# Optimization experiments

Measured on AMD Instinct MI355X. Metric: run time of the kernel, lower is better.

The kernel has to match this reference:

```python
import jax, jax.numpy as jnp
import numpy as np

L, D, H, DK, FF, R, N, B = 8, 256, 8, 32, 1024, 37, 1024, 1
EPS = 1e-6


def setup_inputs() -> dict:
    key = jax.random.key(0)
    ks = jax.random.split(key, 16)
    def w(i, shape, s=0.05):
        return jax.random.normal(ks[i], shape, jnp.float32) * s
    return {
        "x": jax.random.normal(ks[0], (B, N, D), jnp.float32),
        "relations": jax.random.randint(ks[1], (N, N), 0, R),
        "Wq": w(2, (L, D, D)), "bq": jnp.zeros((L, D), jnp.float32),
        "Wk": w(3, (L, D, D)), "bk": jnp.zeros((L, D), jnp.float32),
        "Wv": w(4, (L, D, D)), "bv": jnp.zeros((L, D), jnp.float32),
        "Wo": w(5, (L, D, D)), "bo": jnp.zeros((L, D), jnp.float32),
        "rel_k_emb": w(6, (L, R, DK)), "rel_v_emb": w(7, (L, R, DK)),
        "W1": w(8, (L, D, FF)), "b1": jnp.zeros((L, FF), jnp.float32),
        "W2": w(9, (L, FF, D)), "b2": jnp.zeros((L, D), jnp.float32),
        "ln1_g": jnp.ones((L, D), jnp.float32), "ln1_b": jnp.zeros((L, D), jnp.float32),
        "ln2_g": jnp.ones((L, D), jnp.float32), "ln2_b": jnp.zeros((L, D), jnp.float32),
        "lnf_g": jnp.ones((D,), jnp.float32), "lnf_b": jnp.zeros((D,), jnp.float32),
    }


def _layernorm(h, g, b):
    # Annotated-Transformer LayerNorm: g*(x-mu)/(std+eps)+b with unbiased std
    mu = h.mean(-1, keepdims=True)
    sd = jnp.sqrt(h.var(-1, keepdims=True, ddof=1))
    return g * (h - mu) / (sd + EPS) + b


def reference(x, relations, Wq, bq, Wk, bk, Wv, bv, Wo, bo,
              rel_k_emb, rel_v_emb, W1, b1, W2, b2,
              ln1_g, ln1_b, ln2_g, ln2_b, lnf_g, lnf_b):
    Bb, n, d = x.shape
    scale = 1.0 / jnp.sqrt(jnp.float32(DK))
    for l in range(L):
        # --- relation-aware self-attention sublayer (pre-norm residual) ---
        xn = _layernorm(x, ln1_g[l], ln1_b[l])
        q = (xn @ Wq[l] + bq[l]).reshape(Bb, n, H, DK).transpose(0, 2, 1, 3)
        k = (xn @ Wk[l] + bk[l]).reshape(Bb, n, H, DK).transpose(0, 2, 1, 3)
        v = (xn @ Wv[l] + bv[l]).reshape(Bb, n, H, DK).transpose(0, 2, 1, 3)
        rk = rel_k_emb[l][relations]  # [n, n, DK] irregular gather
        rv = rel_v_emb[l][relations]  # [n, n, DK]
        scores = (jnp.einsum('bhid,bhjd->bhij', q, k)
                  + jnp.einsum('bhid,ijd->bhij', q, rk)) * scale
        p = jax.nn.softmax(scores, axis=-1)
        o = (jnp.einsum('bhij,bhjd->bhid', p, v)
             + jnp.einsum('bhij,ijd->bhid', p, rv))
        o = o.transpose(0, 2, 1, 3).reshape(Bb, n, d) @ Wo[l] + bo[l]
        x = x + o
        # --- position-wise FFN sublayer (pre-norm residual) ---
        xn = _layernorm(x, ln2_g[l], ln2_b[l])
        x = x + (jax.nn.relu(xn @ W1[l] + b1[l]) @ W2[l] + b2[l])
    return _layernorm(x, lnf_g, lnf_b)
```

## Files before the change

kernel.cpp:

```cpp
#include <hip/hip_runtime.h>
#include <stdint.h>

#define L_ 8
#define D_ 256
#define H_ 8
#define DK_ 32
#define FF_ 1024
#define R_ 37
#define N_ 1024
#define JS_ 8

#define SCL (0.17677669529663689f * 1.4426950408889634f)

typedef float f4v __attribute__((ext_vector_type(4)));
typedef short b8v __attribute__((ext_vector_type(8)));
typedef uint  u2v __attribute__((ext_vector_type(2)));

__device__ __forceinline__ ushort f2b(float f){
  union { float f; uint32_t u; } x; x.f = f;
  return (ushort)((x.u + 0x7FFFu + ((x.u >> 16) & 1u)) >> 16);
}
__device__ __forceinline__ float b2f(ushort u){
  union { uint32_t u; float f; } x; x.u = ((uint32_t)u) << 16;
  return x.f;
}
__device__ __forceinline__ uint pk2b(float lo, float hi){
  return (((uint)f2b(hi)) << 16) | (uint)f2b(lo);
}
__device__ __forceinline__ float ex2(float x){ return __builtin_amdgcn_exp2f(x); }

__global__ __launch_bounds__(256)
void wcast_kernel(const float* __restrict__ src, ushort* __restrict__ dst, int K, int Nc){
  __shared__ float t[32][33];
  int l = blockIdx.z;
  long base = (long)l * K * Nc;
  int n0 = blockIdx.x * 32, k0 = blockIdx.y * 32;
  int tx = threadIdx.x, ty = threadIdx.y;
  #pragma unroll
  for (int r = 0; r < 32; r += 8)
    t[ty + r][tx] = src[base + (long)(k0 + ty + r) * Nc + n0 + tx];
  __syncthreads();
  #pragma unroll
  for (int r = 0; r < 32; r += 8)
    dst[base + (long)(n0 + ty + r) * K + k0 + tx] = f2b(t[tx][ty + r]);
}

__global__ __launch_bounds__(256)
void rel8_kernel(const int* __restrict__ rel, uint* __restrict__ rel8){
  long idx = (long)blockIdx.x * 256 + threadIdx.x;
  int4 v = ((const int4*)rel)[idx];
  rel8[idx] = (uint)(v.x & 255) | ((uint)(v.y & 255) << 8)
            | ((uint)(v.z & 255) << 16) | ((uint)(v.w & 255) << 24);
}

template<int OUTB>
__global__ __launch_bounds__(64)
void ln_kernel(const float* __restrict__ x, const float* __restrict__ g, const float* __restrict__ b,
               ushort* __restrict__ ob, float* __restrict__ of){
  int row = blockIdx.x, lane = threadIdx.x;
  float4 v = ((const float4*)(x + (long)row * D_))[lane];
  float s = v.x + v.y + v.z + v.w;
  float s2 = v.x*v.x + v.y*v.y + v.z*v.z + v.w*v.w;
  #pragma unroll
  for (int o = 32; o; o >>= 1){ s += __shfl_xor(s, o); s2 += __shfl_xor(s2, o); }
  float mu = s * (1.f / D_);
  float var = (s2 - D_ * mu * mu) * (1.f / (D_ - 1));
  var = fmaxf(var, 0.f);
  float inv = 1.f / (sqrtf(var) + 1e-6f);
  float4 gv = ((const float4*)g)[lane];
  float4 bv = ((const float4*)b)[lane];
  float o0 = gv.x * (v.x - mu) * inv + bv.x;
  float o1 = gv.y * (v.y - mu) * inv + bv.y;
  float o2 = gv.z * (v.z - mu) * inv + bv.z;
  float o3 = gv.w * (v.w - mu) * inv + bv.w;
  if (OUTB){
    ushort4 u; u.x = f2b(o0); u.y = f2b(o1); u.z = f2b(o2); u.w = f2b(o3);
    ((ushort4*)ob)[(long)row * 64 + lane] = u;
  } else {
    float4 o; o.x = o0; o.y = o1; o.z = o2; o.w = o3;
    ((float4*)of)[(long)row * 64 + lane] = o;
  }
}

template<int QKV, int RELU, int RESID, int OUTF, int OUTB>
__global__ __launch_bounds__(256)
void gemm_kernel(const ushort* __restrict__ A,
                 const ushort* __restrict__ W0, const ushort* __restrict__ W1p, const ushort* __restrict__ W2p,
                 const float* __restrict__ B0, const float* __restrict__ B1p, const float* __restrict__ B2p,
                 float* __restrict__ resid, float* __restrict__ outF, ushort* __restrict__ outB,
                 ushort* __restrict__ outB2,
                 int M, int Nc, int K){
  __shared__ ushort Al[64 * 48];
  __shared__ ushort Bl[64 * 48];
  int tid = threadIdx.x;
  int lane = tid & 63, w = tid >> 6;
  int wm = w >> 1, wn = w & 1;
  int bn0 = blockIdx.x * 64, bm0 = blockIdx.y * 64;
  const ushort* WT; const float* bias; int wn0;
  if (QKV){
    int which = bn0 >> 8;
    WT = which == 0 ? W0 : (which == 1 ? W1p : W2p);
    bias = which == 0 ? B0 : (which == 1 ? B1p : B2p);
    wn0 = bn0 & 255;
  } else { WT = W0; bias = B0; wn0 = bn0; }

  int r4 = tid >> 2, c8 = (tid & 3) * 8;
  const ushort* ag = A + (long)(bm0 + r4) * K + c8;
  const ushort* bg = WT + (long)(wn0 + r4) * K + c8;

  f4v acc[2][2];
  #pragma unroll
  for (int i = 0; i < 2; ++i)
    #pragma unroll
    for (int j = 0; j < 2; ++j)
      acc[i][j] = (f4v){0.f, 0.f, 0.f, 0.f};

  int l16 = lane & 15, lg = lane >> 4;
  int arow0 = (wm * 32 + l16) * 48 + lg * 8;
  int brow0 = (wn * 32 + l16) * 48 + lg * 8;

  for (int k0 = 0; k0 < K; k0 += 32){
    b8v a8 = *(const b8v*)(ag + k0);
    b8v b8 = *(const b8v*)(bg + k0);
    __syncthreads();
    *(b8v*)&Al[r4 * 48 + c8] = a8;
    *(b8v*)&Bl[r4 * 48 + c8] = b8;
    __syncthreads();
    b8v a0 = *(const b8v*)&Al[arow0];
    b8v a1 = *(const b8v*)&Al[arow0 + 16 * 48];
    b8v b0 = *(const b8v*)&Bl[brow0];
    b8v b1 = *(const b8v*)&Bl[brow0 + 16 * 48];
    acc[0][0] = __builtin_amdgcn_mfma_f32_16x16x32_bf16(a0, b0, acc[0][0], 0, 0, 0);
    acc[0][1] = __builtin_amdgcn_mfma_f32_16x16x32_bf16(a0, b1, acc[0][1], 0, 0, 0);
    acc[1][0] = __builtin_amdgcn_mfma_f32_16x16x32_bf16(a1, b0, acc[1][0], 0, 0, 0);
    acc[1][1] = __builtin_amdgcn_mfma_f32_16x16x32_bf16(a1, b1, acc[1][1], 0, 0, 0);
  }
  #pragma unroll
  for (int fi = 0; fi < 2; ++fi)
    #pragma unroll
    for (int fj = 0; fj < 2; ++fj){
      int row0 = bm0 + wm * 32 + fi * 16 + lg * 4;
      int col = bn0 + wn * 32 + fj * 16 + l16;
      float vv[4];
      #pragma unroll
      for (int j = 0; j < 4; ++j) vv[j] = acc[fi][fj][j] + bias[QKV ? (col & 255) : col];
      if (QKV){
        int which = col >> 8, hh = (col >> 5) & 7, dk = col & 31;
        if (which == 2){
          ushort4 pk; pk.x = f2b(vv[0]); pk.y = f2b(vv[1]); pk.z = f2b(vv[2]); pk.w = f2b(vv[3]);
          *(ushort4*)(outB2 + (long)hh * 32768 + (long)dk * 1024 + row0) = pk;
        } else {
          #pragma unroll
          for (int j = 0; j < 4; ++j)
            outB[(long)which * 262144 + (long)hh * 32768 + (long)(row0 + j) * 32 + dk] = f2b(vv[j]);
        }
      } else {
        #pragma unroll
        for (int j = 0; j < 4; ++j){
          float v = vv[j];
          if (RELU) v = fmaxf(v, 0.f);
          long idx = (long)(row0 + j) * Nc + col;
          if (RESID) v += resid[idx];
          if (OUTF) outF[idx] = v;
          if (OUTB) outB[idx] = f2b(v);
        }
      }
    }
}

__global__ __launch_bounds__(320)
void qr_kernel(const ushort* __restrict__ qb, const float* __restrict__ rke, float* __restrict__ qr){
  __shared__ float ql[256];
  int i = blockIdx.x, t = threadIdx.x;
  if (t < 256){
    int h = t >> 5, dk = t & 31;
    ql[t] = b2f(qb[(long)((h << 10) + i) * 32 + dk]);
  }
  __syncthreads();
  if (t < H_ * R_){
    int h = t / R_, r = t - h * R_;
    const float* qh = &ql[h * DK_];
    const float* e = rke + r * DK_;
    float acc = 0.f;
    #pragma unroll
    for (int d = 0; d < DK_; ++d) acc += qh[d] * e[d];
    qr[((long)(h << 10) + i) * 40 + r] = acc * SCL;
  }
}

__global__ __launch_bounds__(256)
void attn_kernel(const ushort* __restrict__ qb, const ushort* __restrict__ kb,
                 const ushort* __restrict__ vbt, const float* __restrict__ qr,
                 const unsigned char* __restrict__ rel8, float* __restrict__ part){
  __shared__ float qr_l[64 * 40];
  __shared__ float prb[64 * 40];
  __shared__ uint  p_l[4 * 16 * 20];

  int tid = threadIdx.x, lane = tid & 63, w = tid >> 6;
  int l16 = lane & 15, g = lane >> 4;
  int ib0 = blockIdx.x * 64, h = blockIdx.y, js = blockIdx.z;
  int i_loc = w * 16 + l16;

  {
    const float* src = qr + (long)((h << 10) + ib0) * 40;
    for (int idx = tid; idx < 2560; idx += 256){ qr_l[idx] = src[idx]; prb[idx] = 0.f; }
  }
  __syncthreads();

  b8v qf = *(const b8v*)(qb + (long)((h << 10) + ib0 + i_loc) * 32 + g * 8);

  f4v oacc0 = (f4v){0.f,0.f,0.f,0.f}, oacc1 = (f4v){0.f,0.f,0.f,0.f};
  float m = -3.0e38f, lsum = 0.f;
  const float* qrr = &qr_l[i_loc * 40];
  float* prr = &prb[i_loc * 40];
  const unsigned char* relrow = rel8 + (long)(ib0 + i_loc) * N_ + js * (N_ / JS_);
  const ushort* kbh = kb + (long)(h << 10) * 32;
  const ushort* vth = vbt + (long)h * 32 * 1024;
  uint* pw = &p_l[w * 320 + l16 * 20];

  #pragma unroll
  for (int jt = 0; jt < N_ / JS_ / 32; ++jt){
    int j0 = js * (N_ / JS_) + jt * 32;
    b8v kf0 = *(const b8v*)(kbh + (long)(j0 + l16) * 32 + g * 8);
    b8v kf1 = *(const b8v*)(kbh + (long)(j0 + 16 + l16) * 32 + g * 8);
    b8v vt0 = *(const b8v*)(vth + (long)l16 * 1024 + j0 + g * 8);
    b8v vt1 = *(const b8v*)(vth + (long)(16 + l16) * 1024 + j0 + g * 8);
    uint rr0 = *(const uint*)(relrow + jt * 32 + g * 4);
    uint rr1 = *(const uint*)(relrow + jt * 32 + 16 + g * 4);

    f4v z = (f4v){0.f,0.f,0.f,0.f};
    f4v s0 = __builtin_amdgcn_mfma_f32_16x16x32_bf16(kf0, qf, z, 0, 0, 0);
    f4v s1 = __builtin_amdgcn_mfma_f32_16x16x32_bf16(kf1, qf, z, 0, 0, 0);

    int rix[8];
    float sv[8];
    #pragma unroll
    for (int e = 0; e < 4; ++e){
      rix[e]     = (rr0 >> (8 * e)) & 255;
      rix[e + 4] = (rr1 >> (8 * e)) & 255;
      sv[e]     = s0[e] * SCL + qrr[rix[e]];
      sv[e + 4] = s1[e] * SCL + qrr[rix[e + 4]];
    }
    float tmax = sv[0];
    #pragma unroll
    for (int e = 1; e < 8; ++e) tmax = fmaxf(tmax, sv[e]);
    tmax = fmaxf(tmax, __shfl_xor(tmax, 16));
    tmax = fmaxf(tmax, __shfl_xor(tmax, 32));

    if (tmax - m > 12.f){
      float f = ex2(m - tmax);
      oacc0 *= f; oacc1 *= f; lsum *= f;
      #pragma unroll
      for (int b2 = 0; b2 < 10; ++b2){
        int bi = g * 10 + b2;
        if (bi < R_) prr[bi] *= f;
      }
      m = tmax;
    }
    float p[8], ps = 0.f;
    #pragma unroll
    for (int e = 0; e < 8; ++e){ p[e] = ex2(sv[e] - m); ps += p[e]; }
    ps += __shfl_xor(ps, 16);
    ps += __shfl_xor(ps, 32);
    lsum += ps;
    #pragma unroll
    for (int e = 0; e < 8; ++e) atomicAdd(&prr[rix[e]], p[e]);

    uint pk0 = pk2b(p[0], p[1]), pk1 = pk2b(p[2], p[3]);
    uint pk2 = pk2b(p[4], p[5]), pk3 = pk2b(p[6], p[7]);
    *(u2v*)&pw[g * 2]     = (u2v){pk0, pk1};
    *(u2v*)&pw[8 + g * 2] = (u2v){pk2, pk3};
    b8v pf = *(const b8v*)&pw[g * 4];
    oacc0 = __builtin_amdgcn_mfma_f32_16x16x32_bf16(vt0, pf, oacc0, 0, 0, 0);
    oacc1 = __builtin_amdgcn_mfma_f32_16x16x32_bf16(vt1, pf, oacc1, 0, 0, 0);
  }

  float* pp = part + ((long)(h * JS_ + js) * N_ + ib0 + i_loc) * 72;
  #pragma unroll
  for (int r2 = 0; r2 < 4; ++r2){
    pp[g * 4 + r2] = oacc0[r2];
    pp[16 + g * 4 + r2] = oacc1[r2];
  }
  #pragma unroll
  for (int b2 = 0; b2 < 10; ++b2){
    int bi = g * 10 + b2;
    if (bi < R_) pp[32 + bi] = prr[bi];
  }
  if (g == 0){ pp[69] = m; pp[70] = lsum; }
}

__global__ __launch_bounds__(256)
void combine_kernel(const float* __restrict__ part, const float* __restrict__ rve,
                    ushort* __restrict__ ob){
  __shared__ float prl[4][40];
  int tid = threadIdx.x, lane = tid & 63, w = tid >> 6;
  int i = blockIdx.x * 4 + w, h = blockIdx.y;
  int d = lane & 31;
  const float* pb = part + ((long)h * JS_) * N_ * 72 + (long)i * 72;
  float ms[JS_], ls[JS_], wf[JS_];
  float mstar = -3.0e38f;
  #pragma unroll
  for (int s = 0; s < JS_; ++s){
    ms[s] = pb[(long)s * N_ * 72 + 69];
    ls[s] = pb[(long)s * N_ * 72 + 70];
    mstar = fmaxf(mstar, ms[s]);
  }
  float lstar = 0.f;
  #pragma unroll
  for (int s = 0; s < JS_; ++s){ wf[s] = ex2(ms[s] - mstar); lstar += ls[s] * wf[s]; }
  float o1d = 0.f;
  #pragma unroll
  for (int s = 0; s < JS_; ++s) o1d += pb[(long)s * N_ * 72 + d] * wf[s];
  if (lane < R_){
    float prv = 0.f;
    #pragma unroll
    for (int s = 0; s < JS_; ++s) prv += pb[(long)s * N_ * 72 + 32 + lane] * wf[s];
    prl[w][lane] = prv;
  }
  float o2 = 0.f;
  for (int r = 0; r < R_; ++r) o2 += prl[w][r] * rve[r * DK_ + d];
  float val = (o1d + o2) / lstar;
  if (lane < 32) ob[(long)i * D_ + h * DK_ + d] = f2b(val);
}

extern "C" void kernel_launch(void* const* d_in, const int* in_sizes, int n_in,
                              void* d_out, int out_size, void* d_ws, size_t ws_size,
                              hipStream_t stream){
  const float* x    = (const float*)d_in[0];
  const int*   rel  = (const int*)d_in[1];
  const float* Wq   = (const float*)d_in[2];
  const float* bq   = (const float*)d_in[3];
  const float* Wk   = (const float*)d_in[4];
  const float* bk   = (const float*)d_in[5];
  const float* Wv   = (const float*)d_in[6];
  const float* bv   = (const float*)d_in[7];
  const float* Wo   = (const float*)d_in[8];
  const float* bo   = (const float*)d_in[9];
  const float* rke  = (const float*)d_in[10];
  const float* rve  = (const float*)d_in[11];
  const float* W1   = (const float*)d_in[12];
  const float* b1   = (const float*)d_in[13];
  const float* W2   = (const float*)d_in[14];
  const float* b2   = (const float*)d_in[15];
  const float* ln1g = (const float*)d_in[16];
  const float* ln1b = (const float*)d_in[17];
  const float* ln2g = (const float*)d_in[18];
  const float* ln2b = (const float*)d_in[19];
  const float* lnfg = (const float*)d_in[20];
  const float* lnfb = (const float*)d_in[21];

  char* wsb = (char*)d_ws;
  size_t off = 0;
  auto alloc = [&](size_t bytes){ void* p = wsb + off; off += (bytes + 255) & ~255ull; return p; };
  float*  xw   = (float*) alloc((size_t)N_ * D_ * 4);
  ushort* qkvb = (ushort*)alloc((size_t)3 * H_ * N_ * DK_ * 2);
  ushort* vbt  = (ushort*)alloc((size_t)H_ * DK_ * N_ * 2);
  float*  qr   = (float*) alloc((size_t)H_ * N_ * 40 * 4);
  ushort* xnb  = (ushort*)alloc((size_t)N_ * D_ * 2);
  ushort* obf  = (ushort*)alloc((size_t)N_ * D_ * 2);
  float*  part = (float*) alloc((size_t)H_ * JS_ * N_ * 72 * 4);
  ushort* hidb = (ushort*)part;
  uint*   rel8 = (uint*)  alloc((size_t)N_ * N_);
  ushort* wqT  = (ushort*)alloc((size_t)L_ * D_ * D_ * 2);
  ushort* wkT  = (ushort*)alloc((size_t)L_ * D_ * D_ * 2);
  ushort* wvT  = (ushort*)alloc((size_t)L_ * D_ * D_ * 2);
  ushort* woT  = (ushort*)alloc((size_t)L_ * D_ * D_ * 2);
  ushort* w1T  = (ushort*)alloc((size_t)L_ * D_ * FF_ * 2);
  ushort* w2T  = (ushort*)alloc((size_t)L_ * D_ * FF_ * 2);
  (void)ws_size; (void)in_sizes; (void)n_in; (void)out_size;

  ushort* qb = qkvb;
  ushort* kb = qkvb + (size_t)H_ * N_ * DK_;

  dim3 tb(32, 8);
  wcast_kernel<<<dim3(D_/32,  D_/32,  L_), tb, 0, stream>>>(Wq, wqT, D_, D_);
  wcast_kernel<<<dim3(D_/32,  D_/32,  L_), tb, 0, stream>>>(Wk, wkT, D_, D_);
  wcast_kernel<<<dim3(D_/32,  D_/32,  L_), tb, 0, stream>>>(Wv, wvT, D_, D_);
  wcast_kernel<<<dim3(D_/32,  D_/32,  L_), tb, 0, stream>>>(Wo, woT, D_, D_);
  wcast_kernel<<<dim3(FF_/32, D_/32,  L_), tb, 0, stream>>>(W1, w1T, D_, FF_);
  wcast_kernel<<<dim3(D_/32,  FF_/32, L_), tb, 0, stream>>>(W2, w2T, FF_, D_);
  rel8_kernel<<<N_ * N_ / 1024, 256, 0, stream>>>(rel, rel8);

  hipMemcpyAsync(xw, x, (size_t)N_ * D_ * 4, hipMemcpyDeviceToDevice, stream);

  for (int l = 0; l < L_; ++l){
    ln_kernel<1><<<N_, 64, 0, stream>>>(xw, ln1g + l * D_, ln1b + l * D_, xnb, nullptr);
    gemm_kernel<1,0,0,0,1><<<dim3(768/64, N_/64), 256, 0, stream>>>(
        xnb, wqT + (size_t)l * D_ * D_, wkT + (size_t)l * D_ * D_, wvT + (size_t)l * D_ * D_,
        bq + l * D_, bk + l * D_, bv + l * D_,
        nullptr, nullptr, qkvb, vbt, N_, 768, D_);
    qr_kernel<<<N_, 320, 0, stream>>>(qb, rke + (size_t)l * R_ * DK_, qr);
    attn_kernel<<<dim3(N_/64, H_, JS_), 256, 0, stream>>>(qb, kb, vbt, qr, (const unsigned char*)rel8, part);
    combine_kernel<<<dim3(N_/4, H_), 256, 0, stream>>>(part, rve + (size_t)l * R_ * DK_, obf);
    gemm_kernel<0,0,1,1,0><<<dim3(D_/64, N_/64), 256, 0, stream>>>(
        obf, woT + (size_t)l * D_ * D_, nullptr, nullptr,
        bo + l * D_, nullptr, nullptr,
        xw, xw, nullptr, nullptr, N_, D_, D_);
    ln_kernel<1><<<N_, 64, 0, stream>>>(xw, ln2g + l * D_, ln2b + l * D_, xnb, nullptr);
    gemm_kernel<0,1,0,0,1><<<dim3(FF_/64, N_/64), 256, 0, stream>>>(
        xnb, w1T + (size_t)l * D_ * FF_, nullptr, nullptr,
        b1 + l * FF_, nullptr, nullptr,
        nullptr, nullptr, hidb, nullptr, N_, FF_, D_);
    gemm_kernel<0,0,1,1,0><<<dim3(D_/64, N_/64), 256, 0, stream>>>(
        hidb, w2T + (size_t)l * FF_ * D_, nullptr, nullptr,
        b2 + l * D_, nullptr, nullptr,
        xw, xw, nullptr, nullptr, N_, D_, FF_);
  }
  ln_kernel<0><<<N_, 64, 0, stream>>>(xw, lnfg, lnfb, nullptr, (float*)d_out);
}
```

Measured before the change: 871.9 us.

## Fuse q·rel_k, attention, and split-K combine into one attention kernel

```diff
diff --git a/kernel.cpp b/kernel.cpp
--- a/kernel.cpp
+++ b/kernel.cpp
@@ -8,7 +8,7 @@
 #define FF_ 1024
 #define R_ 37
 #define N_ 1024
-#define JS_ 8
+#define AIB 32
 
 #define SCL (0.17677669529663689f * 1.4426950408889634f)
 
@@ -168,59 +168,63 @@
     }
 }
 
-__global__ __launch_bounds__(320)
-void qr_kernel(const ushort* __restrict__ qb, const float* __restrict__ rke, float* __restrict__ qr){
-  __shared__ float ql[256];
-  int i = blockIdx.x, t = threadIdx.x;
-  if (t < 256){
-    int h = t >> 5, dk = t & 31;
-    ql[t] = b2f(qb[(long)((h << 10) + i) * 32 + dk]);
-  }
-  __syncthreads();
-  if (t < H_ * R_){
-    int h = t / R_, r = t - h * R_;
-    const float* qh = &ql[h * DK_];
-    const float* e = rke + r * DK_;
-    float acc = 0.f;
-    #pragma unroll
-    for (int d = 0; d < DK_; ++d) acc += qh[d] * e[d];
-    qr[((long)(h << 10) + i) * 40 + r] = acc * SCL;
-  }
-}
-
-__global__ __launch_bounds__(256)
+__global__ __launch_bounds__(512)
 void attn_kernel(const ushort* __restrict__ qb, const ushort* __restrict__ kb,
-                 const ushort* __restrict__ vbt, const float* __restrict__ qr,
-                 const unsigned char* __restrict__ rel8, float* __restrict__ part){
-  __shared__ float qr_l[64 * 40];
-  __shared__ float prb[64 * 40];
-  __shared__ uint  p_l[4 * 16 * 20];
+                 const ushort* __restrict__ vbt, const float* __restrict__ rke,
+                 const float* __restrict__ rve,
+                 const unsigned char* __restrict__ rel8, ushort* __restrict__ ob){
+  __shared__ float q_l[AIB * 32];
+  __shared__ float qr_l[AIB * 40];
+  __shared__ float prb[4 * AIB * 40];
+  __shared__ uint  p_l[8 * 16 * 20];
+  __shared__ float part_l[4 * AIB * 34];
+  __shared__ float wf_l[4 * AIB];
+  __shared__ float lrow_l[AIB];
 
   int tid = threadIdx.x, lane = tid & 63, w = tid >> 6;
   int l16 = lane & 15, g = lane >> 4;
-  int ib0 = blockIdx.x * 64, h = blockIdx.y, js = blockIdx.z;
-  int i_loc = w * 16 + l16;
-
-  {
-    const float* src = qr + (long)((h << 10) + ib0) * 40;
-    for (int idx = tid; idx < 2560; idx += 256){ qr_l[idx] = src[idx]; prb[idx] = 0.f; }
-  }
-  __syncthreads();
-
-  b8v qf = *(const b8v*)(qb + (long)((h << 10) + ib0 + i_loc) * 32 + g * 8);
+  int ib0 = blockIdx.x * AIB, h = blockIdx.y;
+  int js = w >> 1, ig = w & 1;
+  int ir = ig * 16 + l16;
+
+  if (tid < 256){
+    int row = tid >> 3, d4 = (tid & 7) * 4;
+    ushort4 u = *(const ushort4*)(qb + (long)((h << 10) + ib0 + row) * 32 + d4);
+    q_l[row * 32 + d4 + 0] = b2f(u.x);
+    q_l[row * 32 + d4 + 1] = b2f(u.y);
+    q_l[row * 32 + d4 + 2] = b2f(u.z);
+    q_l[row * 32 + d4 + 3] = b2f(u.w);
+  }
+  for (int idx = tid; idx < 4 * AIB * 40; idx += 512) prb[idx] = 0.f;
+  __syncthreads();
+
+  for (int slot = tid; slot < AIB * 40; slot += 512){
+    int row = slot / 40, r = slot - row * 40;
+    if (r < R_){
+      const float* qh = &q_l[row * 32];
+      const float* e = rke + r * 32;
+      float acc = 0.f;
+      #pragma unroll
+      for (int d = 0; d < 32; ++d) acc += qh[d] * e[d];
+      qr_l[slot] = acc * SCL;
+    }
+  }
+  __syncthreads();
+
+  b8v qf = *(const b8v*)(qb + (long)((h << 10) + ib0 + ir) * 32 + g * 8);
 
   f4v oacc0 = (f4v){0.f,0.f,0.f,0.f}, oacc1 = (f4v){0.f,0.f,0.f,0.f};
   float m = -3.0e38f, lsum = 0.f;
-  const float* qrr = &qr_l[i_loc * 40];
-  float* prr = &prb[i_loc * 40];
-  const unsigned char* relrow = rel8 + (long)(ib0 + i_loc) * N_ + js * (N_ / JS_);
+  const float* qrr = &qr_l[ir * 40];
+  float* prr = &prb[(js * AIB + ir) * 40];
+  const unsigned char* relrow = rel8 + (long)(ib0 + ir) * N_ + js * 256;
   const ushort* kbh = kb + (long)(h << 10) * 32;
   const ushort* vth = vbt + (long)h * 32 * 1024;
   uint* pw = &p_l[w * 320 + l16 * 20];
 
   #pragma unroll
-  for (int jt = 0; jt < N_ / JS_ / 32; ++jt){
-    int j0 = js * (N_ / JS_) + jt * 32;
+  for (int jt = 0; jt < 8; ++jt){
+    int j0 = js * 256 + jt * 32;
     b8v kf0 = *(const b8v*)(kbh + (long)(j0 + l16) * 32 + g * 8);
     b8v kf1 = *(const b8v*)(kbh + (long)(j0 + 16 + l16) * 32 + g * 8);
     b8v vt0 = *(const b8v*)(vth + (long)l16 * 1024 + j0 + g * 8);
@@ -275,52 +279,58 @@
     oacc1 = __builtin_amdgcn_mfma_f32_16x16x32_bf16(vt1, pf, oacc1, 0, 0, 0);
   }
 
-  float* pp = part + ((long)(h * JS_ + js) * N_ + ib0 + i_loc) * 72;
-  #pragma unroll
-  for (int r2 = 0; r2 < 4; ++r2){
-    pp[g * 4 + r2] = oacc0[r2];
-    pp[16 + g * 4 + r2] = oacc1[r2];
-  }
-  #pragma unroll
-  for (int b2 = 0; b2 < 10; ++b2){
-    int bi = g * 10 + b2;
-    if (bi < R_) pp[32 + bi] = prr[bi];
-  }
-  if (g == 0){ pp[69] = m; pp[70] = lsum; }
-}
-
-__global__ __launch_bounds__(256)
-void combine_kernel(const float* __restrict__ part, const float* __restrict__ rve,
-                    ushort* __restrict__ ob){
-  __shared__ float prl[4][40];
-  int tid = threadIdx.x, lane = tid & 63, w = tid >> 6;
-  int i = blockIdx.x * 4 + w, h = blockIdx.y;
-  int d = lane & 31;
-  const float* pb = part + ((long)h * JS_) * N_ * 72 + (long)i * 72;
-  float ms[JS_], ls[JS_], wf[JS_];
-  float mstar = -3.0e38f;
-  #pragma unroll
-  for (int s = 0; s < JS_; ++s){
-    ms[s] = pb[(long)s * N_ * 72 + 69];
-    ls[s] = pb[(long)s * N_ * 72 + 70];
-    mstar = fmaxf(mstar, ms[s]);
-  }
-  float lstar = 0.f;
-  #pragma unroll
-  for (int s = 0; s < JS_; ++s){ wf[s] = ex2(ms[s] - mstar); lstar += ls[s] * wf[s]; }
-  float o1d = 0.f;
-  #pragma unroll
-  for (int s = 0; s < JS_; ++s) o1d += pb[(long)s * N_ * 72 + d] * wf[s];
-  if (lane < R_){
-    float prv = 0.f;
-    #pragma unroll
-    for (int s = 0; s < JS_; ++s) prv += pb[(long)s * N_ * 72 + 32 + lane] * wf[s];
-    prl[w][lane] = prv;
-  }
-  float o2 = 0.f;
-  for (int r = 0; r < R_; ++r) o2 += prl[w][r] * rve[r * DK_ + d];
-  float val = (o1d + o2) / lstar;
-  if (lane < 32) ob[(long)i * D_ + h * DK_ + d] = f2b(val);
+  {
+    float* pp = &part_l[(js * AIB + ir) * 34];
+    #pragma unroll
+    for (int e = 0; e < 4; ++e){
+      pp[g * 4 + e] = oacc0[e];
+      pp[16 + g * 4 + e] = oacc1[e];
+    }
+    if (g == 0){ pp[32] = m; pp[33] = lsum; }
+  }
+  __syncthreads();
+
+  if (tid < AIB){
+    int row = tid;
+    float ms[4], ls[4];
+    float mstar = -3.0e38f;
+    #pragma unroll
+    for (int s = 0; s < 4; ++s){
+      ms[s] = part_l[(s * AIB + row) * 34 + 32];
+      ls[s] = part_l[(s * AIB + row) * 34 + 33];
+      mstar = fmaxf(mstar, ms[s]);
+    }
+    float lstar = 0.f;
+    #pragma unroll
+    for (int s = 0; s < 4; ++s){
+      float wfv = ex2(ms[s] - mstar);
+      wf_l[s * AIB + row] = wfv;
+      lstar += ls[s] * wfv;
+    }
+    lrow_l[row] = lstar;
+  }
+  __syncthreads();
+
+  for (int slot = tid; slot < AIB * 40; slot += 512){
+    int row = slot / 40;
+    float acc = 0.f;
+    #pragma unroll
+    for (int s = 0; s < 4; ++s) acc += prb[(s * AIB) * 40 + slot] * wf_l[s * AIB + row];
+    prb[slot] = acc;
+  }
+  __syncthreads();
+
+  for (int slot = tid; slot < AIB * 32; slot += 512){
+    int row = slot >> 5, d = slot & 31;
+    float o1 = 0.f;
+    #pragma unroll
+    for (int s = 0; s < 4; ++s) o1 += part_l[(s * AIB + row) * 34 + d] * wf_l[s * AIB + row];
+    float o2 = 0.f;
+    #pragma unroll
+    for (int r = 0; r < R_; ++r) o2 += prb[row * 40 + r] * rve[r * 32 + d];
+    float val = (o1 + o2) / lrow_l[row];
+    ob[(long)(ib0 + row) * D_ + h * 32 + d] = f2b(val);
+  }
 }
 
 extern "C" void kernel_launch(void* const* d_in, const int* in_sizes, int n_in,
@@ -355,11 +365,9 @@
   float*  xw   = (float*) alloc((size_t)N_ * D_ * 4);
   ushort* qkvb = (ushort*)alloc((size_t)3 * H_ * N_ * DK_ * 2);
   ushort* vbt  = (ushort*)alloc((size_t)H_ * DK_ * N_ * 2);
-  float*  qr   = (float*) alloc((size_t)H_ * N_ * 40 * 4);
   ushort* xnb  = (ushort*)alloc((size_t)N_ * D_ * 2);
   ushort* obf  = (ushort*)alloc((size_t)N_ * D_ * 2);
-  float*  part = (float*) alloc((size_t)H_ * JS_ * N_ * 72 * 4);
-  ushort* hidb = (ushort*)part;
+  ushort* hidb = (ushort*)alloc((size_t)N_ * FF_ * 2);
   uint*   rel8 = (uint*)  alloc((size_t)N_ * N_);
   ushort* wqT  = (ushort*)alloc((size_t)L_ * D_ * D_ * 2);
   ushort* wkT  = (ushort*)alloc((size_t)L_ * D_ * D_ * 2);
@@ -389,9 +397,9 @@
         xnb, wqT + (size_t)l * D_ * D_, wkT + (size_t)l * D_ * D_, wvT + (size_t)l * D_ * D_,
         bq + l * D_, bk + l * D_, bv + l * D_,
         nullptr, nullptr, qkvb, vbt, N_, 768, D_);
-    qr_kernel<<<N_, 320, 0, stream>>>(qb, rke + (size_t)l * R_ * DK_, qr);
-    attn_kernel<<<dim3(N_/64, H_, JS_), 256, 0, stream>>>(qb, kb, vbt, qr, (const unsigned char*)rel8, part);
-    combine_kernel<<<dim3(N_/4, H_), 256, 0, stream>>>(part, rve + (size_t)l * R_ * DK_, obf);
+    attn_kernel<<<dim3(N_/AIB, H_), 512, 0, stream>>>(
+        qb, kb, vbt, rke + (size_t)l * R_ * DK_, rve + (size_t)l * R_ * DK_,
+        (const unsigned char*)rel8, obf);
     gemm_kernel<0,0,1,1,0><<<dim3(D_/64, N_/64), 256, 0, stream>>>(
         obf, woT + (size_t)l * D_ * D_, nullptr, nullptr,
         bo + l * D_, nullptr, nullptr,
```

Result: faster. 787.8 us (-9.6%).

## Split fused flash attention into materialized QK GEMM, softmax, and PV GEMM kernels

Applied to the files above, without the earlier changes.

```diff
diff --git a/kernel.cpp b/kernel.cpp
--- a/kernel.cpp
+++ b/kernel.cpp
@@ -8,13 +8,11 @@
 #define FF_ 1024
 #define R_ 37
 #define N_ 1024
-#define JS_ 8
 
 #define SCL (0.17677669529663689f * 1.4426950408889634f)
 
 typedef float f4v __attribute__((ext_vector_type(4)));
 typedef short b8v __attribute__((ext_vector_type(8)));
-typedef uint  u2v __attribute__((ext_vector_type(2)));
 
 __device__ __forceinline__ ushort f2b(float f){
   union { float f; uint32_t u; } x; x.f = f;
@@ -24,10 +22,19 @@
   union { uint32_t u; float f; } x; x.u = ((uint32_t)u) << 16;
   return x.f;
 }
-__device__ __forceinline__ uint pk2b(float lo, float hi){
-  return (((uint)f2b(hi)) << 16) | (uint)f2b(lo);
+__device__ __forceinline__ ushort f2h(float f){
+  union { _Float16 h; ushort u; } x; x.h = (_Float16)f;
+  return x.u;
+}
+__device__ __forceinline__ float h2f(ushort u){
+  union { ushort u; _Float16 h; } x; x.u = u;
+  return (float)x.h;
 }
 __device__ __forceinline__ float ex2(float x){ return __builtin_amdgcn_exp2f(x); }
+
+__device__ __forceinline__ void lds_fadd(float* p, float v){
+  asm volatile("ds_add_f32 %0, %1" :: "v"((uint)(uintptr_t)p), "v"(v) : "memory");
+}
 
 __global__ __launch_bounds__(256)
 void wcast_kernel(const float* __restrict__ src, ushort* __restrict__ dst, int K, int Nc){
@@ -82,20 +89,22 @@
   }
 }
 
-template<int QKV, int RELU, int RESID, int OUTF, int OUTB>
+template<int QKV, int RELU, int RESID, int OUTF, int OUTB, int OUTH = 0>
 __global__ __launch_bounds__(256)
 void gemm_kernel(const ushort* __restrict__ A,
                  const ushort* __restrict__ W0, const ushort* __restrict__ W1p, const ushort* __restrict__ W2p,
                  const float* __restrict__ B0, const float* __restrict__ B1p, const float* __restrict__ B2p,
                  float* __restrict__ resid, float* __restrict__ outF, ushort* __restrict__ outB,
                  ushort* __restrict__ outB2,
-                 int M, int Nc, int K){
+                 int M, int Nc, int K, long aB, long wB, long oB){
   __shared__ ushort Al[64 * 48];
   __shared__ ushort Bl[64 * 48];
   int tid = threadIdx.x;
   int lane = tid & 63, w = tid >> 6;
   int wm = w >> 1, wn = w & 1;
   int bn0 = blockIdx.x * 64, bm0 = blockIdx.y * 64;
+  long zb = blockIdx.z;
+  A += zb * aB;
   const ushort* WT; const float* bias; int wn0;
   if (QKV){
     int which = bn0 >> 8;
@@ -103,6 +112,7 @@
     bias = which == 0 ? B0 : (which == 1 ? B1p : B2p);
     wn0 = bn0 & 255;
   } else { WT = W0; bias = B0; wn0 = bn0; }
+  WT += zb * wB;
 
   int r4 = tid >> 2, c8 = (tid & 3) * 8;
   const ushort* ag = A + (long)(bm0 + r4) * K + c8;
@@ -141,6 +151,13 @@
     for (int fj = 0; fj < 2; ++fj){
       int row0 = bm0 + wm * 32 + fi * 16 + lg * 4;
       int col = bn0 + wn * 32 + fj * 16 + l16;
+      if (OUTH){
+        ushort4 pk;
+        pk.x = f2h(acc[fi][fj][0]); pk.y = f2h(acc[fi][fj][1]);
+        pk.z = f2h(acc[fi][fj][2]); pk.w = f2h(acc[fi][fj][3]);
+        *(ushort4*)(outB + zb * oB + (long)col * 1024 + row0) = pk;
+        continue;
+      }
       float vv[4];
       #pragma unroll
       for (int j = 0; j < 4; ++j) vv[j] = acc[fi][fj][j] + bias[QKV ? (col & 255) : col];
@@ -189,138 +206,109 @@
 }
 
 __global__ __launch_bounds__(256)
-void attn_kernel(const ushort* __restrict__ qb, const ushort* __restrict__ kb,
-                 const ushort* __restrict__ vbt, const float* __restrict__ qr,
-                 const unsigned char* __restrict__ rel8, float* __restrict__ part){
-  __shared__ float qr_l[64 * 40];
-  __shared__ float prb[64 * 40];
-  __shared__ uint  p_l[4 * 16 * 20];
-
+void sm_kernel(const ushort* __restrict__ S, const float* __restrict__ qr,
+               const unsigned char* __restrict__ rel8, const float* __restrict__ rve,
+               ushort* __restrict__ P, float* __restrict__ o2){
+  __shared__ float qrl[4][40];
+  __shared__ float bins[4][44];
+  int tid = threadIdx.x, lane = tid & 63, w = tid >> 6;
+  int h = blockIdx.y, i = blockIdx.x * 4 + w;
+  long rowq = (long)(h << 10) + i;
+
+  if (lane < 40) qrl[w][lane] = qr[rowq * 40 + lane];
+  if (lane < 44) bins[w][lane] = 0.f;
+
+  const ushort* Srow = S + rowq * 1024 + lane * 16;
+  b8v s0 = *(const b8v*)Srow;
+  b8v s1 = *(const b8v*)(Srow + 8);
+  uint4 rr = *(const uint4*)(rel8 + (long)i * 1024 + lane * 16);
+  uint rw[4] = { rr.x, rr.y, rr.z, rr.w };
+
+  int rix[16];
+  #pragma unroll
+  for (int q = 0; q < 4; ++q)
+    #pragma unroll
+    for (int e = 0; e < 4; ++e)
+      rix[q * 4 + e] = (rw[q] >> (8 * e)) & 255;
+
+  float sv[16];
+  #pragma unroll
+  for (int e = 0; e < 8; ++e){
+    sv[e]     = h2f((ushort)s0[e]) * SCL + qrl[w][rix[e]];
+    sv[8 + e] = h2f((ushort)s1[e]) * SCL + qrl[w][rix[8 + e]];
+  }
+  float m = sv[0];
+  #pragma unroll
+  for (int e = 1; e < 16; ++e) m = fmaxf(m, sv[e]);
+  #pragma unroll
+  for (int o = 1; o < 64; o <<= 1) m = fmaxf(m, __shfl_xor(m, o));
+
+  float p[16], ls = 0.f;
+  #pragma unroll
+  for (int e = 0; e < 16; ++e){ p[e] = ex2(sv[e] - m); ls += p[e]; }
+  #pragma unroll
+  for (int o = 1; o < 64; o <<= 1) ls += __shfl_xor(ls, o);
+  float rinv = 1.f / ls;
+
+  #pragma unroll
+  for (int e = 0; e < 16; ++e) lds_fadd(&bins[w][rix[e]], p[e]);
+
+  b8v po0, po1;
+  #pragma unroll
+  for (int e = 0; e < 8; ++e){
+    po0[e] = (short)f2b(p[e] * rinv);
+    po1[e] = (short)f2b(p[8 + e] * rinv);
+  }
+  *(b8v*)(P + rowq * 1024 + lane * 16) = po0;
+  *(b8v*)(P + rowq * 1024 + lane * 16 + 8) = po1;
+
+  int d = lane & 31, half = lane >> 5;
+  float acc = 0.f;
+  int r0 = half * 19, r1 = r0 + 19 < R_ ? r0 + 19 : R_;
+  for (int r = r0; r < r1; ++r) acc += bins[w][r] * rve[r * 32 + d];
+  acc += __shfl_xor(acc, 32);
+  if (lane < 32) o2[rowq * 32 + d] = acc * rinv;
+}
+
+__global__ __launch_bounds__(256)
+void pv_kernel(const ushort* __restrict__ P, const ushort* __restrict__ vbt,
+               const float* __restrict__ o2, ushort* __restrict__ ob){
+  __shared__ ushort Al[64 * 48];
+  __shared__ ushort Bl[32 * 48];
   int tid = threadIdx.x, lane = tid & 63, w = tid >> 6;
   int l16 = lane & 15, g = lane >> 4;
-  int ib0 = blockIdx.x * 64, h = blockIdx.y, js = blockIdx.z;
-  int i_loc = w * 16 + l16;
-
-  {
-    const float* src = qr + (long)((h << 10) + ib0) * 40;
-    for (int idx = tid; idx < 2560; idx += 256){ qr_l[idx] = src[idx]; prb[idx] = 0.f; }
-  }
-  __syncthreads();
-
-  b8v qf = *(const b8v*)(qb + (long)((h << 10) + ib0 + i_loc) * 32 + g * 8);
-
-  f4v oacc0 = (f4v){0.f,0.f,0.f,0.f}, oacc1 = (f4v){0.f,0.f,0.f,0.f};
-  float m = -3.0e38f, lsum = 0.f;
-  const float* qrr = &qr_l[i_loc * 40];
-  float* prr = &prb[i_loc * 40];
-  const unsigned char* relrow = rel8 + (long)(ib0 + i_loc) * N_ + js * (N_ / JS_);
-  const ushort* kbh = kb + (long)(h << 10) * 32;
-  const ushort* vth = vbt + (long)h * 32 * 1024;
-  uint* pw = &p_l[w * 320 + l16 * 20];
-
-  #pragma unroll
-  for (int jt = 0; jt < N_ / JS_ / 32; ++jt){
-    int j0 = js * (N_ / JS_) + jt * 32;
-    b8v kf0 = *(const b8v*)(kbh + (long)(j0 + l16) * 32 + g * 8);
-    b8v kf1 = *(const b8v*)(kbh + (long)(j0 + 16 + l16) * 32 + g * 8);
-    b8v vt0 = *(const b8v*)(vth + (long)l16 * 1024 + j0 + g * 8);
-    b8v vt1 = *(const b8v*)(vth + (long)(16 + l16) * 1024 + j0 + g * 8);
-    uint rr0 = *(const uint*)(relrow + jt * 32 + g * 4);
-    uint rr1 = *(const uint*)(relrow + jt * 32 + 16 + g * 4);
-
-    f4v z = (f4v){0.f,0.f,0.f,0.f};
-    f4v s0 = __builtin_amdgcn_mfma_f32_16x16x32_bf16(kf0, qf, z, 0, 0, 0);
-    f4v s1 = __builtin_amdgcn_mfma_f32_16x16x32_bf16(kf1, qf, z, 0, 0, 0);
-
-    int rix[8];
-    float sv[8];
-    #pragma unroll
-    for (int e = 0; e < 4; ++e){
-      rix[e]     = (rr0 >> (8 * e)) & 255;
-      rix[e + 4] = (rr1 >> (8 * e)) & 255;
-      sv[e]     = s0[e] * SCL + qrr[rix[e]];
-      sv[e + 4] = s1[e] * SCL + qrr[rix[e + 4]];
-    }
-    float tmax = sv[0];
-    #pragma unroll
-    for (int e = 1; e < 8; ++e) tmax = fmaxf(tmax, sv[e]);
-    tmax = fmaxf(tmax, __shfl_xor(tmax, 16));
-    tmax = fmaxf(tmax, __shfl_xor(tmax, 32));
-
-    if (tmax - m > 12.f){
-      float f = ex2(m - tmax);
-      oacc0 *= f; oacc1 *= f; lsum *= f;
-      #pragma unroll
-      for (int b2 = 0; b2 < 10; ++b2){
-        int bi = g * 10 + b2;
-        if (bi < R_) prr[bi] *= f;
-      }
-      m = tmax;
-    }
-    float p[8], ps = 0.f;
-    #pragma unroll
-    for (int e = 0; e < 8; ++e){ p[e] = ex2(sv[e] - m); ps += p[e]; }
-    ps += __shfl_xor(ps, 16);
-    ps += __shfl_xor(ps, 32);
-    lsum += ps;
-    #pragma unroll
-    for (int e = 0; e < 8; ++e) atomicAdd(&prr[rix[e]], p[e]);
-
-    uint pk0 = pk2b(p[0], p[1]), pk1 = pk2b(p[2], p[3]);
-    uint pk2 = pk2b(p[4], p[5]), pk3 = pk2b(p[6], p[7]);
-    *(u2v*)&pw[g * 2]     = (u2v){pk0, pk1};
-    *(u2v*)&pw[8 + g * 2] = (u2v){pk2, pk3};
-    b8v pf = *(const b8v*)&pw[g * 4];
-    oacc0 = __builtin_amdgcn_mfma_f32_16x16x32_bf16(vt0, pf, oacc0, 0, 0, 0);
-    oacc1 = __builtin_amdgcn_mfma_f32_16x16x32_bf16(vt1, pf, oacc1, 0, 0, 0);
-  }
-
-  float* pp = part + ((long)(h * JS_ + js) * N_ + ib0 + i_loc) * 72;
-  #pragma unroll
-  for (int r2 = 0; r2 < 4; ++r2){
-    pp[g * 4 + r2] = oacc0[r2];
-    pp[16 + g * 4 + r2] = oacc1[r2];
-  }
-  #pragma unroll
-  for (int b2 = 0; b2 < 10; ++b2){
-    int bi = g * 10 + b2;
-    if (bi < R_) pp[32 + bi] = prr[bi];
-  }
-  if (g == 0){ pp[69] = m; pp[70] = lsum; }
-}
-
-__global__ __launch_bounds__(256)
-void combine_kernel(const float* __restrict__ part, const float* __restrict__ rve,
-                    ushort* __restrict__ ob){
-  __shared__ float prl[4][40];
-  int tid = threadIdx.x, lane = tid & 63, w = tid >> 6;
-  int i = blockIdx.x * 4 + w, h = blockIdx.y;
-  int d = lane & 31;
-  const float* pb = part + ((long)h * JS_) * N_ * 72 + (long)i * 72;
-  float ms[JS_], ls[JS_], wf[JS_];
-  float mstar = -3.0e38f;
-  #pragma unroll
-  for (int s = 0; s < JS_; ++s){
-    ms[s] = pb[(long)s * N_ * 72 + 69];
-    ls[s] = pb[(long)s * N_ * 72 + 70];
-    mstar = fmaxf(mstar, ms[s]);
-  }
-  float lstar = 0.f;
-  #pragma unroll
-  for (int s = 0; s < JS_; ++s){ wf[s] = ex2(ms[s] - mstar); lstar += ls[s] * wf[s]; }
-  float o1d = 0.f;
-  #pragma unroll
-  for (int s = 0; s < JS_; ++s) o1d += pb[(long)s * N_ * 72 + d] * wf[s];
-  if (lane < R_){
-    float prv = 0.f;
-    #pragma unroll
-    for (int s = 0; s < JS_; ++s) prv += pb[(long)s * N_ * 72 + 32 + lane] * wf[s];
-    prl[w][lane] = prv;
-  }
-  float o2 = 0.f;
-  for (int r = 0; r < R_; ++r) o2 += prl[w][r] * rve[r * DK_ + d];
-  float val = (o1d + o2) / lstar;
-  if (lane < 32) ob[(long)i * D_ + h * DK_ + d] = f2b(val);
+  int i0 = blockIdx.x * 64, h = blockIdx.y;
+  const ushort* Ph = P + (long)h * 1024 * 1024;
+  const ushort* Vh = vbt + (long)h * 32 * 1024;
+  int r4 = tid >> 2, c8 = (tid & 3) * 8;
+
+  f4v acc0 = (f4v){0,0,0,0}, acc1 = (f4v){0,0,0,0};
+  int arow = (w * 16 + l16) * 48 + g * 8;
+  int brow0 = l16 * 48 + g * 8, brow1 = (16 + l16) * 48 + g * 8;
+
+  for (int k0 = 0; k0 < 1024; k0 += 32){
+    b8v a8 = *(const b8v*)(Ph + (long)(i0 + r4) * 1024 + k0 + c8);
+    b8v b8;
+    if (tid < 128) b8 = *(const b8v*)(Vh + (long)r4 * 1024 + k0 + c8);
+    __syncthreads();
+    *(b8v*)&Al[r4 * 48 + c8] = a8;
+    if (tid < 128) *(b8v*)&Bl[r4 * 48 + c8] = b8;
+    __syncthreads();
+    b8v a0 = *(const b8v*)&Al[arow];
+    b8v b0 = *(const b8v*)&Bl[brow0];
+    b8v b1 = *(const b8v*)&Bl[brow1];
+    acc0 = __builtin_amdgcn_mfma_f32_16x16x32_bf16(a0, b0, acc0, 0, 0, 0);
+    acc1 = __builtin_amdgcn_mfma_f32_16x16x32_bf16(a0, b1, acc1, 0, 0, 0);
+  }
+  #pragma unroll
+  for (int e = 0; e < 4; ++e){
+    int i = i0 + w * 16 + g * 4 + e;
+    long ob2 = ((long)(h << 10) + i) * 32;
+    float v0 = acc0[e] + o2[ob2 + l16];
+    float v1 = acc1[e] + o2[ob2 + 16 + l16];
+    ob[(long)i * 256 + h * 32 + l16] = f2b(v0);
+    ob[(long)i * 256 + h * 32 + 16 + l16] = f2b(v1);
+  }
 }
 
 extern "C" void kernel_launch(void* const* d_in, const int* in_sizes, int n_in,
@@ -358,9 +346,11 @@
   float*  qr   = (float*) alloc((size_t)H_ * N_ * 40 * 4);
   ushort* xnb  = (ushort*)alloc((size_t)N_ * D_ * 2);
   ushort* obf  = (ushort*)alloc((size_t)N_ * D_ * 2);
-  float*  part = (float*) alloc((size_t)H_ * JS_ * N_ * 72 * 4);
-  ushort* hidb = (ushort*)part;
+  ushort* hidb = (ushort*)alloc((size_t)N_ * FF_ * 2);
   uint*   rel8 = (uint*)  alloc((size_t)N_ * N_);
+  ushort* Sbuf = (ushort*)alloc((size_t)H_ * N_ * N_ * 2);
+  ushort* Pbuf = (ushort*)alloc((size_t)H_ * N_ * N_ * 2);
+  float*  o2b  = (float*) alloc((size_t)H_ * N_ * DK_ * 4);
   ushort* wqT  = (ushort*)alloc((size_t)L_ * D_ * D_ * 2);
   ushort* wkT  = (ushort*)alloc((size_t)L_ * D_ * D_ * 2);
   ushort* wvT  = (ushort*)alloc((size_t)L_ * D_ * D_ * 2);
@@ -388,23 +378,28 @@
     gemm_kernel<1,0,0,0,1><<<dim3(768/64, N_/64), 256, 0, stream>>>(
         xnb, wqT + (size_t)l * D_ * D_, wkT + (size_t)l * D_ * D_, wvT + (size_t)l * D_ * D_,
         bq + l * D_, bk + l * D_, bv + l * D_,
-        nullptr, nullptr, qkvb, vbt, N_, 768, D_);
+        nullptr, nullptr, qkvb, vbt, N_, 768, D_, 0, 0, 0);
     qr_kernel<<<N_, 320, 0, stream>>>(qb, rke + (size_t)l * R_ * DK_, qr);
-    attn_kernel<<<dim3(N_/64, H_, JS_), 256, 0, stream>>>(qb, kb, vbt, qr, (const unsigned char*)rel8, part);
-    combine_kernel<<<dim3(N_/4, H_), 256, 0, stream>>>(part, rve + (size_t)l * R_ * DK_, obf);
+    gemm_kernel<0,0,0,0,0,1><<<dim3(N_/64, N_/64, H_), 256, 0, stream>>>(
+        kb, qb, nullptr, nullptr, nullptr, nullptr, nullptr,
+        nullptr, nullptr, Sbuf, nullptr, N_, N_, DK_,
+        (long)N_ * DK_, (long)N_ * DK_, (long)N_ * N_);
+    sm_kernel<<<dim3(N_/4, H_), 256, 0, stream>>>(
+        Sbuf, qr, (const unsigned char*)rel8, rve + (size_t)l * R_ * DK_, Pbuf, o2b);
+    pv_kernel<<<dim3(N_/64, H_), 256, 0, stream>>>(Pbuf, vbt, o2b, obf);
     gemm_kernel<0,0,1,1,0><<<dim3(D_/64, N_/64), 256, 0, stream>>>(
         obf, woT + (size_t)l * D_ * D_, nullptr, nullptr,
         bo + l * D_, nullptr, nullptr,
-        xw, xw, nullptr, nullptr, N_, D_, D_);
+        xw, xw, nullptr, nullptr, N_, D_, D_, 0, 0, 0);
     ln_kernel<1><<<N_, 64, 0, stream>>>(xw, ln2g + l * D_, ln2b + l * D_, xnb, nullptr);
     gemm_kernel<0,1,0,0,1><<<dim3(FF_/64, N_/64), 256, 0, stream>>>(
         xnb, w1T + (size_t)l * D_ * FF_, nullptr, nullptr,
         b1 + l * FF_, nullptr, nullptr,
-        nullptr, nullptr, hidb, nullptr, N_, FF_, D_);
+        nullptr, nullptr, hidb, nullptr, N_, FF_, D_, 0, 0, 0);
     gemm_kernel<0,0,1,1,0><<<dim3(D_/64, N_/64), 256, 0, stream>>>(
         hidb, w2T + (size_t)l * FF_ * D_, nullptr, nullptr,
         b2 + l * D_, nullptr, nullptr,
-        xw, xw, nullptr, nullptr, N_, D_, FF_);
+        xw, xw, nullptr, nullptr, N_, D_, FF_, 0, 0, 0);
   }
   ln_kernel<0><<<N_, 64, 0, stream>>>(xw, lnfg, lnfb, nullptr, (float*)d_out);
 }
```

Result: slower. 943.2 us (+8.2%).
